# Kernel tuning notes

Measured on AMD Instinct MI355X. Metric: run time of the kernel, lower is better.

## Reference

```python
import jax, jax.numpy as jnp
import numpy as np

N = 100000      # nodes
E = 3200000     # edges (avg degree 32)
NODE, EDGE, H = 11, 2, 32
EPS = 1e-5


def setup_inputs() -> dict:
    key = jax.random.key(0)
    ks = jax.random.split(key, 12)
    def w(k, shape):  # small init like torch Linear
        return jax.random.normal(k, shape, dtype=jnp.float32) * 0.1
    inp = {
        'x': jax.random.normal(ks[0], (N, NODE), dtype=jnp.float32),
        'edge_attr': jax.random.normal(ks[1], (E, EDGE), dtype=jnp.float32),
        'edge_index': jax.random.randint(ks[2], (2, E), 0, N),
        # mlp1: Lin(13,32)-BN-ReLU-Lin(32,32)-BN-ReLU
        'w1a': w(ks[3], (NODE + EDGE, H)), 'b1a': jnp.zeros(H), 'g1a': jnp.ones(H), 'be1a': jnp.zeros(H),
        'w1b': w(ks[4], (H, H)),           'b1b': jnp.zeros(H), 'g1b': jnp.ones(H), 'be1b': jnp.zeros(H),
        # mlp2: Lin(43,32)-BN-ReLU then Lin(32,1)-ReLU (no BN on last)
        'w2a': w(ks[5], (NODE + H, H)), 'b2a': jnp.zeros(H), 'g2a': jnp.ones(H), 'be2a': jnp.zeros(H),
        'w2b': w(ks[6], (H, 1)),        'b2b': jnp.zeros(1),
        # power: Lin(11,32)-BN-ReLU-Lin(32,1)-BN-ReLU
        'wpa': w(ks[7], (NODE, H)), 'bpa': jnp.zeros(H), 'gpa': jnp.ones(H), 'bepa': jnp.zeros(H),
        'wpb': w(ks[8], (H, 1)),    'bpb': jnp.zeros(1), 'gpb': jnp.ones(1), 'bepb': jnp.zeros(1),
    }
    return inp


def _bn(x, g, b):
    # training-mode BatchNorm1d (batch stats, biased variance), like torch default
    mu = x.mean(0, keepdims=True)
    var = ((x - mu) ** 2).mean(0, keepdims=True)
    return (x - mu) * jax.lax.rsqrt(var + EPS) * g + b


def _conv(x, edge_index, edge_attr,
          w1a, b1a, g1a, be1a, w1b, b1b, g1b, be1b,
          w2a, b2a, g2a, be2a, w2b, b2b):
    src, dst = edge_index[0], edge_index[1]
    # message: cat([x_j, edge_attr]) -> mlp1
    m = jnp.concatenate([x[src], edge_attr], axis=1)          # [E, 13]
    m = jax.nn.relu(_bn(m @ w1a + b1a, g1a, be1a))            # [E, 32]
    m = jax.nn.relu(_bn(m @ w1b + b1b, g1b, be1b))            # [E, 32]
    # aggr='max' scatter to destination nodes
    agg = jax.ops.segment_max(m, dst, num_segments=x.shape[0])
    agg = jnp.where(jnp.isneginf(agg), 0.0, agg)              # empty segments -> 0
    # update: cat([x, aggr_out]) -> mlp2, then replace last feature column
    h = jax.nn.relu(_bn(jnp.concatenate([x, agg], axis=1) @ w2a + b2a, g2a, be2a))
    comb = jax.nn.relu(h @ w2b + b2b)                         # [N, 1]
    return jnp.concatenate([x[:, :-1], comb], axis=1)         # [N, 11]


def reference(x, edge_attr, edge_index,
              w1a, b1a, g1a, be1a, w1b, b1b, g1b, be1b,
              w2a, b2a, g2a, be2a, w2b, b2b,
              wpa, bpa, gpa, bepa, wpb, bpb, gpb, bepb):
    for _ in range(3):
        x = _conv(x, edge_index, edge_attr,
                  w1a, b1a, g1a, be1a, w1b, b1b, g1b, be1b,
                  w2a, b2a, g2a, be2a, w2b, b2b)
    h = jax.nn.relu(_bn(x @ wpa + bpa, gpa, bepa))
    out = jax.nn.relu(_bn(h @ wpb + bpb, gpb, bepb))
    return out
```

## Files before the change

kernel.cpp:

```cpp
#include <hip/hip_runtime.h>
#include <hip/hip_bf16.h>
#include <cstddef>

#define NN 100000
#define EE 3200000
#define NBIN 64
static const float EF = 3200000.0f;


__device__ __forceinline__ float wsum(float v) {
  #pragma unroll
  for (int off = 32; off > 0; off >>= 1) v += __shfl_down(v, off, 64);
  return v;
}

__device__ __forceinline__ void reduce64(float sum[32], float ssq[32], float* red,
                                         float* __restrict__ gsum, float* __restrict__ gssq) {
  const int wid = threadIdx.x >> 6, lane = threadIdx.x & 63;
  #pragma unroll
  for (int j = 0; j < 32; j++) {
    float a = wsum(sum[j]);
    float b = wsum(ssq[j]);
    if (lane == 0) { red[wid * 64 + j] = a; red[wid * 64 + 32 + j] = b; }
  }
  __syncthreads();
  if (threadIdx.x < 64) {
    float t = red[threadIdx.x] + red[64 + threadIdx.x] + red[128 + threadIdx.x] + red[192 + threadIdx.x];
    if (threadIdx.x < 32) unsafeAtomicAdd(&gsum[threadIdx.x], t);
    else                  unsafeAtomicAdd(&gssq[threadIdx.x - 32], t);
  }
}

__device__ __forceinline__ void loadrow(const float* __restrict__ xp, int s, float in[13]) {
  const float4* xr = reinterpret_cast<const float4*>(xp + (size_t)s * 12);
  float4 r0 = xr[0], r1 = xr[1], r2 = xr[2];
  in[0]=r0.x; in[1]=r0.y; in[2]=r0.z; in[3]=r0.w; in[4]=r1.x; in[5]=r1.y; in[6]=r1.z; in[7]=r1.w;
  in[8]=r2.x; in[9]=r2.y; in[10]=r2.z;
}

__device__ __forceinline__ unsigned long long packsea(float x, float y) {
  unsigned int xq = (unsigned int)(fmaf(x, 16384.f, 131072.f) + 0.5f);
  unsigned int yq = (unsigned int)(fmaf(y, 16384.f, 131072.f) + 0.5f);
  return (1ULL << 54) | ((unsigned long long)yq << 27) | (unsigned long long)xq;
}


__global__ __launch_bounds__(256) void k_wprep(const float* __restrict__ w1b,
    const float* __restrict__ b1b, const float* __restrict__ g1b,
    const float* __restrict__ w2a, const float* __restrict__ b2a,
    const float* __restrict__ wpa, const float* __restrict__ bpa,
    float* __restrict__ w2tf, float* __restrict__ b1bf,
    float* __restrict__ w2aT, float* __restrict__ wpaT) {
  int t = threadIdx.x;
  for (int i = t; i < 1024; i += 256) {
    int j = i >> 5, k = i & 31;
    float d = (g1b[j] >= 0.f) ? 1.f : -1.f;
    w2tf[j * 32 + k] = d * w1b[k * 32 + j];
  }
  for (int i = t; i < 32 * 43; i += 256) { int j = i & 31, k = i >> 5; w2aT[j * 44 + k] = w2a[k * 32 + j]; }
  for (int i = t; i < 32 * 11; i += 256) { int j = i & 31, k = i >> 5; wpaT[j * 12 + k] = wpa[k * 32 + j]; }
  if (t < 32) {
    float d = (g1b[t] >= 0.f) ? 1.f : -1.f;
    b1bf[t] = d * b1b[t];
    w2aT[t * 44 + 43] = b2a[t];
    wpaT[t * 12 + 11] = bpa[t];
  }
}

__global__ __launch_bounds__(256) void k_prep(const int* __restrict__ dst, const int* __restrict__ src,
    const float* __restrict__ ea, int* __restrict__ cnt, int* __restrict__ rank,
    unsigned long long* __restrict__ nsd, float* __restrict__ cmom) {
  float p0 = 0, p1 = 0, p2 = 0, p3 = 0, p4 = 0;
  const int S = gridDim.x * 256;
  for (int g = blockIdx.x * 256 + threadIdx.x; g < EE / 4; g += S) {
    int4 d4 = reinterpret_cast<const int4*>(dst)[g];
    int4 s4 = reinterpret_cast<const int4*>(src)[g];
    float4 e0 = reinterpret_cast<const float4*>(ea)[2 * g];
    float4 e1 = reinterpret_cast<const float4*>(ea)[2 * g + 1];
    int r0 = atomicAdd(&cnt[d4.x], 1);
    int r1 = atomicAdd(&cnt[d4.y], 1);
    int r2 = atomicAdd(&cnt[d4.z], 1);
    int r3 = atomicAdd(&cnt[d4.w], 1);
    reinterpret_cast<int4*>(rank)[g] = make_int4(r0, r1, r2, r3);
    atomicAdd(&nsd[s4.x], packsea(e0.x, e0.y));
    atomicAdd(&nsd[s4.y], packsea(e0.z, e0.w));
    atomicAdd(&nsd[s4.z], packsea(e1.x, e1.y));
    atomicAdd(&nsd[s4.w], packsea(e1.z, e1.w));
    p0 += e0.x * e0.x + e0.z * e0.z + e1.x * e1.x + e1.z * e1.z;
    p1 += e0.x * e0.y + e0.z * e0.w + e1.x * e1.y + e1.z * e1.w;
    p2 += e0.y * e0.y + e0.w * e0.w + e1.y * e1.y + e1.w * e1.w;
    p3 += e0.x + e0.z + e1.x + e1.z;
    p4 += e0.y + e0.w + e1.y + e1.w;
  }
  p0 = wsum(p0); p1 = wsum(p1); p2 = wsum(p2); p3 = wsum(p3); p4 = wsum(p4);
  if ((threadIdx.x & 63) == 0) {
    unsafeAtomicAdd(&cmom[0], p0); unsafeAtomicAdd(&cmom[1], p1); unsafeAtomicAdd(&cmom[2], p2);
    unsafeAtomicAdd(&cmom[3], p3); unsafeAtomicAdd(&cmom[4], p4);
  }
}

__global__ __launch_bounds__(1024) void k_scan(const int* __restrict__ cnt,
                                               int* __restrict__ starts) {
  __shared__ int part[1024];
  const int T = 1024, CH = (NN + T - 1) / T;
  int t = threadIdx.x;
  int lo = t * CH, hi = min(lo + CH, NN);
  int s = 0;
  for (int i = lo; i < hi; i++) s += cnt[i];
  part[t] = s; __syncthreads();
  for (int off = 1; off < T; off <<= 1) {
    int v = (t >= off) ? part[t - off] : 0;
    __syncthreads();
    part[t] += v;
    __syncthreads();
  }
  int run = part[t] - s;
  for (int i = lo; i < hi; i++) { starts[i] = run; run += cnt[i]; }
  if (t == T - 1) starts[NN] = EE;
}

__global__ __launch_bounds__(256) void k_scatter(const int* __restrict__ dst, const int* __restrict__ src,
    const float* __restrict__ ea, const int* __restrict__ starts, const int* __restrict__ rank,
    int4* __restrict__ edg) {
  const int S = gridDim.x * 256;
  for (int g = blockIdx.x * 256 + threadIdx.x; g < EE / 4; g += S) {
    int4 d4 = reinterpret_cast<const int4*>(dst)[g];
    int4 s4 = reinterpret_cast<const int4*>(src)[g];
    int4 r4 = reinterpret_cast<const int4*>(rank)[g];
    float4 e0 = reinterpret_cast<const float4*>(ea)[2 * g];
    float4 e1 = reinterpret_cast<const float4*>(ea)[2 * g + 1];
    edg[starts[d4.x] + r4.x] = make_int4(s4.x, __float_as_int(e0.x), __float_as_int(e0.y), 0);
    edg[starts[d4.y] + r4.y] = make_int4(s4.y, __float_as_int(e0.z), __float_as_int(e0.w), 0);
    edg[starts[d4.z] + r4.z] = make_int4(s4.z, __float_as_int(e1.x), __float_as_int(e1.y), 0);
    edg[starts[d4.w] + r4.w] = make_int4(s4.w, __float_as_int(e1.z), __float_as_int(e1.w), 0);
  }
}

__global__ __launch_bounds__(256) void k_xp(const float* __restrict__ x, float* __restrict__ xp) {
  int n = blockIdx.x * 256 + threadIdx.x;
  if (n >= NN) return;
  float v[11];
  #pragma unroll
  for (int k = 0; k < 11; k++) v[k] = x[(size_t)n * 11 + k];
  float4* o = reinterpret_cast<float4*>(xp + (size_t)n * 12);
  o[0] = make_float4(v[0], v[1], v[2], v[3]);
  o[1] = make_float4(v[4], v[5], v[6], v[7]);
  o[2] = make_float4(v[8], v[9], v[10], 0.f);
}

__global__ __launch_bounds__(256) void k_mom(const float* __restrict__ xp,
                                             const unsigned long long* __restrict__ nsd,
                                             float* __restrict__ mom) {
  const int n = blockIdx.x * 256 + threadIdx.x;
  const int lane = threadIdx.x & 63;
  float v[11]; float w = 0.f; float sx = 0.f, sy = 0.f;
  #pragma unroll
  for (int k = 0; k < 11; k++) v[k] = 0.f;
  if (n < NN) {
    unsigned long long pv = nsd[n];
    float dg = (float)(unsigned int)(pv >> 54);
    float sxf = (float)(unsigned int)(pv & 0x7FFFFFFull);
    float syf = (float)(unsigned int)((pv >> 27) & 0x7FFFFFFull);
    w = dg;
    sx = sxf * (1.f / 16384.f) - 8.f * dg;
    sy = syf * (1.f / 16384.f) - 8.f * dg;
    loadrow(xp, n, v);
  }
  int ch = 0;
  #pragma unroll
  for (int a = 0; a < 11; a++) {
    float r = wsum(w * v[a]);
    if (lane == 0) unsafeAtomicAdd(&mom[ch], r);
    ch++;
  }
  #pragma unroll
  for (int a = 0; a < 11; a++) {
    #pragma unroll
    for (int b = a; b < 11; b++) {
      float r = wsum(w * v[a] * v[b]);
      if (lane == 0) unsafeAtomicAdd(&mom[ch], r);
      ch++;
    }
  }
  #pragma unroll
  for (int a = 0; a < 11; a++) {
    float rx = wsum(v[a] * sx);
    if (lane == 0) unsafeAtomicAdd(&mom[ch], rx);
    ch++;
    float ry = wsum(v[a] * sy);
    if (lane == 0) unsafeAtomicAdd(&mom[ch], ry);
    ch++;
  }
}

__device__ __forceinline__ float msym(const float* mom, const float* cmom, int k, int l) {
  int a = min(k, l), b = max(k, l);
  if (b < 11) return mom[11 + a * 11 - a * (a - 1) / 2 + (b - a)];
  if (a < 11) return mom[77 + a * 2 + (b - 11)];
  return cmom[(a - 11) + (b - 11)];
}

__global__ void k_fin1(float* __restrict__ mom, const float* __restrict__ cmom,
    const float* __restrict__ w1a, const float* __restrict__ b1a,
    const float* __restrict__ g1a, const float* __restrict__ be1a,
    float* __restrict__ w1f, float* __restrict__ wexy) {
  int j = threadIdx.x;
  float w[13], S[13];
  #pragma unroll
  for (int k = 0; k < 13; k++) w[k] = w1a[k * 32 + j];
  #pragma unroll
  for (int k = 0; k < 11; k++) S[k] = mom[k];
  S[11] = cmom[3]; S[12] = cmom[4];
  float lin = 0.f;
  #pragma unroll
  for (int k = 0; k < 13; k++) lin = fmaf(w[k], S[k], lin);
  float quad = 0.f;
  #pragma unroll
  for (int k = 0; k < 13; k++)
    #pragma unroll
    for (int l = 0; l < 13; l++) quad = fmaf(w[k] * w[l], msym(mom, cmom, k, l), quad);
  const float invE = 1.f / EF;
  float b = b1a[j];
  float mean = fmaf(lin, invE, b);
  float ey2 = (quad + 2.f * b * lin) * invE + b * b;
  float var = fmaxf(ey2 - mean * mean, 0.f);
  float A = g1a[j] * rsqrtf(var + 1e-5f);
  float C = be1a[j] - mean * A;
  #pragma unroll
  for (int k = 0; k < 13; k++) w1f[j * 16 + k] = A * w[k];
  w1f[j * 16 + 13] = fmaf(A, b, C);
  w1f[j * 16 + 14] = 0.f; w1f[j * 16 + 15] = 0.f;
  wexy[j] = A * w[11];
  wexy[32 + j] = A * w[12];
  __syncthreads();
  for (int i = j; i < 128; i += 32) mom[i] = 0.f;
}

__global__ __launch_bounds__(256) void k_P(const float* __restrict__ xp, const float* __restrict__ w1f,
                                           float* __restrict__ P) {
  const int n = blockIdx.x * 256 + threadIdx.x;
  if (n >= NN) return;
  float xv[11];
  loadrow(xp, n, xv);
  float4* op = reinterpret_cast<float4*>(P + (size_t)n * 32);
  #pragma unroll
  for (int jj = 0; jj < 8; jj++) {
    float o[4];
    #pragma unroll
    for (int u = 0; u < 4; u++) {
      int j = 4 * jj + u;
      const float* wr = w1f + j * 16;
      float acc = wr[13];
      #pragma unroll
      for (int k = 0; k < 11; k++) acc = fmaf(xv[k], wr[k], acc);
      o[u] = acc;
    }
    op[jj] = make_float4(o[0], o[1], o[2], o[3]);
  }
}

__global__ __launch_bounds__(256, 6) void k_fusedagg(
    const int* __restrict__ starts, const int4* __restrict__ edg,
    const float* __restrict__ P, const float* __restrict__ wexy,
    const float* __restrict__ w2tf, const float* __restrict__ b1bf,
    float* __restrict__ tzb, float* __restrict__ gms, float* __restrict__ gzq) {
  __shared__ float smx[4][2][32];
  __shared__ float redm[4][32], redq[4][32];
  const int tid = threadIdx.x;
  const int wid = tid >> 6, lane = tid & 63;
  const int half = lane >> 5, l = lane & 31;
  const int c0 = l & 15, h = (l >> 4) & 1;
  const int n = blockIdx.x * 8 + wid * 2 + half;
  const float wex = wexy[l], wey = wexy[32 + l], bz = b1bf[l];
  const float4* wcA = reinterpret_cast<const float4*>(w2tf + (size_t)c0 * 32 + 16 * h);
  const float4* wcB = reinterpret_cast<const float4*>(w2tf + (size_t)(c0 + 16) * 32 + 16 * h);
  const float4 a0 = wcA[0], a1 = wcA[1], a2 = wcA[2], a3 = wcA[3];
  const float4 b0 = wcB[0], b1 = wcB[1], b2 = wcB[2], b3 = wcB[3];
  float tz = -3.0e38f, zq = 0.f, ms = 0.f;
  int lo = 0, hi = 0;
  if (n < NN) { lo = starts[n]; hi = starts[n + 1]; }
  float* msl = &smx[wid][half][0];
  const float* mrd = msl + 16 * h;
  int sl = lo;
  int4 eA = make_int4(0, 0, 0, 0), eB = make_int4(0, 0, 0, 0);
  float pA = 0.f;
  if (sl < hi) {
    eA = edg[sl];
    pA = P[(size_t)eA.x * 32 + l];
  }
  if (sl + 1 < hi) eB = edg[sl + 1];
  while (sl < hi) {
    int4 eC = eB;
    if (sl + 2 < hi) eC = edg[sl + 2];
    float pN = pA;
    if (sl + 1 < hi) pN = P[(size_t)eB.x * 32 + l];
    const float ex = __int_as_float(eA.y), ey = __int_as_float(eA.z);
    const float m = fmaxf(0.f, fmaf(ex, wex, fmaf(ey, wey, pA)));
    ms += m;
    msl[l] = m;
    __builtin_amdgcn_wave_barrier();
    const float4 m0 = *reinterpret_cast<const float4*>(mrd + 0);
    const float4 m1 = *reinterpret_cast<const float4*>(mrd + 4);
    const float4 m2 = *reinterpret_cast<const float4*>(mrd + 8);
    const float4 m3 = *reinterpret_cast<const float4*>(mrd + 12);
    __builtin_amdgcn_wave_barrier();
    float zA0 = 0.f, zA1 = 0.f, zB0 = 0.f, zB1 = 0.f;
    zA0 = fmaf(m0.x, a0.x, zA0); zA1 = fmaf(m0.y, a0.y, zA1);
    zA0 = fmaf(m0.z, a0.z, zA0); zA1 = fmaf(m0.w, a0.w, zA1);
    zA0 = fmaf(m1.x, a1.x, zA0); zA1 = fmaf(m1.y, a1.y, zA1);
    zA0 = fmaf(m1.z, a1.z, zA0); zA1 = fmaf(m1.w, a1.w, zA1);
    zA0 = fmaf(m2.x, a2.x, zA0); zA1 = fmaf(m2.y, a2.y, zA1);
    zA0 = fmaf(m2.z, a2.z, zA0); zA1 = fmaf(m2.w, a2.w, zA1);
    zA0 = fmaf(m3.x, a3.x, zA0); zA1 = fmaf(m3.y, a3.y, zA1);
    zA0 = fmaf(m3.z, a3.z, zA0); zA1 = fmaf(m3.w, a3.w, zA1);
    zB0 = fmaf(m0.x, b0.x, zB0); zB1 = fmaf(m0.y, b0.y, zB1);
    zB0 = fmaf(m0.z, b0.z, zB0); zB1 = fmaf(m0.w, b0.w, zB1);
    zB0 = fmaf(m1.x, b1.x, zB0); zB1 = fmaf(m1.y, b1.y, zB1);
    zB0 = fmaf(m1.z, b1.z, zB0); zB1 = fmaf(m1.w, b1.w, zB1);
    zB0 = fmaf(m2.x, b2.x, zB0); zB1 = fmaf(m2.y, b2.y, zB1);
    zB0 = fmaf(m2.z, b2.z, zB0); zB1 = fmaf(m2.w, b2.w, zB1);
    zB0 = fmaf(m3.x, b3.x, zB0); zB1 = fmaf(m3.y, b3.y, zB1);
    zB0 = fmaf(m3.z, b3.z, zB0); zB1 = fmaf(m3.w, b3.w, zB1);
    float pAh = zA0 + zA1;
    float pBh = zB0 + zB1;
    pAh += __shfl_xor(pAh, 16, 64);
    pBh += __shfl_xor(pBh, 16, 64);
    const float z = ((l & 16) ? pBh : pAh) + bz;
    tz = fmaxf(tz, z);
    zq = fmaf(z, z, zq);
    eA = eB; eB = eC; pA = pN;
    ++sl;
  }
  if (n < NN) tzb[(size_t)n * 32 + l] = tz;
  float msT = ms + __shfl_xor(ms, 32, 64);
  float zqT = zq + __shfl_xor(zq, 32, 64);
  if (lane < 32) { redm[wid][l] = msT; redq[wid][l] = zqT; }
  __syncthreads();
  if (tid < 32) {
    float a = redm[0][tid] + redm[1][tid] + redm[2][tid] + redm[3][tid];
    float b = redq[0][tid] + redq[1][tid] + redq[2][tid] + redq[3][tid];
    const int bin = blockIdx.x & (NBIN - 1);
    unsafeAtomicAdd(&gms[bin * 32 + tid], a);
    unsafeAtomicAdd(&gzq[bin * 32 + tid], b);
  }
}

__global__ void k_fin2(float* __restrict__ gms, float* __restrict__ gzq,
    const float* __restrict__ w1b, const float* __restrict__ b1b,
    const float* __restrict__ g1b, const float* __restrict__ be1b,
    float* __restrict__ A2d, float* __restrict__ C2) {
  __shared__ float sm[32];
  int j = threadIdx.x;
  float msj = 0.f, zqj = 0.f;
  for (int b = 0; b < NBIN; b++) { msj += gms[b * 32 + j]; zqj += gzq[b * 32 + j]; }
  sm[j] = msj;
  __syncthreads();
  float zs = EF * b1b[j];
  #pragma unroll
  for (int k = 0; k < 32; k++) zs = fmaf(w1b[k * 32 + j], sm[k], zs);
  const float invE = 1.f / EF;
  float mu = zs * invE;
  float var = fmaxf(zqj * invE - mu * mu, 0.f);
  float A = g1b[j] * rsqrtf(var + 1e-5f);
  float C = be1b[j] - mu * A;
  float d = (g1b[j] >= 0.f) ? 1.f : -1.f;
  A2d[j] = A * d; C2[j] = C;
  for (int b = 0; b < NBIN; b++) { gms[b * 32 + j] = 0.f; gzq[b * 32 + j] = 0.f; }
}

__global__ void k_finalize(float* __restrict__ sum, float* __restrict__ ssq,
                           const float* __restrict__ g, const float* __restrict__ be,
                           float inv_n, int ncols, float* __restrict__ a, float* __restrict__ c) {
  int j = threadIdx.x;
  if (j < ncols) {
    float mu = sum[j] * inv_n;
    float var = fmaxf(ssq[j] * inv_n - mu * mu, 0.f);
    float s = rsqrtf(var + 1e-5f) * g[j];
    a[j] = s; c[j] = be[j] - mu * s;
    sum[j] = 0.f; ssq[j] = 0.f;
  }
}


__global__ __launch_bounds__(256) void k_hpre2(const float* __restrict__ xp,
    const float* __restrict__ tzb, const int* __restrict__ starts,
    const float* __restrict__ A2d, const float* __restrict__ C2, const float* __restrict__ w2aT,
    float* __restrict__ hpre, float* __restrict__ gsum, float* __restrict__ gssq) {
  __shared__ float red[256];
  const int n = blockIdx.x * 256 + threadIdx.x;
  float h[32], hh[32];
  #pragma unroll
  for (int j = 0; j < 32; j++) h[j] = 0.f;
  if (n < NN) {
    float xv[11];
    loadrow(xp, n, xv);
    const int dg = starts[n + 1] - starts[n];
    float av[32];
    if (dg > 0) {
      const float4* tp = reinterpret_cast<const float4*>(tzb + (size_t)n * 32);
      #pragma unroll
      for (int j = 0; j < 8; j++) {
        float4 v = tp[j];
        av[4 * j]     = fmaxf(0.f, fmaf(A2d[4 * j],     v.x, C2[4 * j]));
        av[4 * j + 1] = fmaxf(0.f, fmaf(A2d[4 * j + 1], v.y, C2[4 * j + 1]));
        av[4 * j + 2] = fmaxf(0.f, fmaf(A2d[4 * j + 2], v.z, C2[4 * j + 2]));
        av[4 * j + 3] = fmaxf(0.f, fmaf(A2d[4 * j + 3], v.w, C2[4 * j + 3]));
      }
    } else {
      #pragma unroll
      for (int j = 0; j < 32; j++) av[j] = 0.f;
    }
    #pragma unroll
    for (int j = 0; j < 32; j++) {
      const float* wr = w2aT + j * 44;
      float acc = wr[43];
      #pragma unroll
      for (int k = 0; k < 11; k++) acc = fmaf(xv[k], wr[k], acc);
      #pragma unroll
      for (int k = 0; k < 32; k++) acc = fmaf(av[k], wr[11 + k], acc);
      h[j] = acc;
    }
    float4* hp = reinterpret_cast<float4*>(hpre + (size_t)n * 32);
    #pragma unroll
    for (int j = 0; j < 8; j++)
      hp[j] = make_float4(h[4 * j], h[4 * j + 1], h[4 * j + 2], h[4 * j + 3]);
  }
  #pragma unroll
  for (int j = 0; j < 32; j++) hh[j] = h[j] * h[j];
  reduce64(h, hh, red, gsum, gssq);
}

__global__ __launch_bounds__(256) void k_comb(const float* __restrict__ hpre,
    const float* __restrict__ a3, const float* __restrict__ c3,
    const float* __restrict__ w2b, const float* __restrict__ b2b, float* __restrict__ xp) {
  const int n = blockIdx.x * 256 + threadIdx.x;
  if (n >= NN) return;
  const float4* hp = reinterpret_cast<const float4*>(hpre + (size_t)n * 32);
  float acc = b2b[0];
  #pragma unroll
  for (int j = 0; j < 8; j++) {
    float4 v = hp[j];
    acc += fmaxf(0.f, fmaf(v.x, a3[4 * j],     c3[4 * j]))     * w2b[4 * j];
    acc += fmaxf(0.f, fmaf(v.y, a3[4 * j + 1], c3[4 * j + 1])) * w2b[4 * j + 1];
    acc += fmaxf(0.f, fmaf(v.z, a3[4 * j + 2], c3[4 * j + 2])) * w2b[4 * j + 2];
    acc += fmaxf(0.f, fmaf(v.w, a3[4 * j + 3], c3[4 * j + 3])) * w2b[4 * j + 3];
  }
  xp[(size_t)n * 12 + 10] = fmaxf(acc, 0.f);
}


__global__ __launch_bounds__(256) void k_p5(const float* __restrict__ xp, const float* __restrict__ wpaT,
                                            float* __restrict__ ybuf,
                                            float* __restrict__ gsum, float* __restrict__ gssq) {
  __shared__ float red[256];
  const int n = blockIdx.x * 256 + threadIdx.x;
  float y[32], yy[32];
  #pragma unroll
  for (int j = 0; j < 32; j++) y[j] = 0.f;
  if (n < NN) {
    float xv[11];
    loadrow(xp, n, xv);
    #pragma unroll
    for (int j = 0; j < 32; j++) {
      const float* wr = wpaT + j * 12;
      float acc = wr[11];
      #pragma unroll
      for (int k = 0; k < 11; k++) acc = fmaf(xv[k], wr[k], acc);
      y[j] = acc;
    }
    float4* yp = reinterpret_cast<float4*>(ybuf + (size_t)n * 32);
    #pragma unroll
    for (int j = 0; j < 8; j++)
      yp[j] = make_float4(y[4 * j], y[4 * j + 1], y[4 * j + 2], y[4 * j + 3]);
  }
  #pragma unroll
  for (int j = 0; j < 32; j++) yy[j] = y[j] * y[j];
  reduce64(y, yy, red, gsum, gssq);
}

__global__ __launch_bounds__(256) void k_p6(const float* __restrict__ ybuf,
    const float* __restrict__ a4, const float* __restrict__ c4,
    const float* __restrict__ wpb, const float* __restrict__ bpb,
    float* __restrict__ yq, float* __restrict__ gsum, float* __restrict__ gssq) {
  __shared__ float red[8];
  const int n = blockIdx.x * 256 + threadIdx.x;
  float sum = 0.f, ssq = 0.f;
  if (n < NN) {
    const float4* yp = reinterpret_cast<const float4*>(ybuf + (size_t)n * 32);
    float q = bpb[0];
    #pragma unroll
    for (int j = 0; j < 8; j++) {
      float4 v = yp[j];
      q = fmaf(fmaxf(0.f, fmaf(v.x, a4[4 * j],     c4[4 * j])),     wpb[4 * j],     q);
      q = fmaf(fmaxf(0.f, fmaf(v.y, a4[4 * j + 1], c4[4 * j + 1])), wpb[4 * j + 1], q);
      q = fmaf(fmaxf(0.f, fmaf(v.z, a4[4 * j + 2], c4[4 * j + 2])), wpb[4 * j + 2], q);
      q = fmaf(fmaxf(0.f, fmaf(v.w, a4[4 * j + 3], c4[4 * j + 3])), wpb[4 * j + 3], q);
    }
    yq[n] = q;
    sum = q; ssq = q * q;
  }
  float s = wsum(sum), qq = wsum(ssq);
  const int wid = threadIdx.x >> 6, lane = threadIdx.x & 63;
  if (lane == 0) { red[wid] = s; red[4 + wid] = qq; }
  __syncthreads();
  if (threadIdx.x == 0) {
    unsafeAtomicAdd(&gsum[0], red[0] + red[1] + red[2] + red[3]);
    unsafeAtomicAdd(&gssq[0], red[4] + red[5] + red[6] + red[7]);
  }
}

__global__ __launch_bounds__(256) void k_p7(const float* __restrict__ yq,
    const float* __restrict__ a5, const float* __restrict__ c5, float* __restrict__ out) {
  int n = blockIdx.x * 256 + threadIdx.x;
  if (n < NN) out[n] = fmaxf(0.f, fmaf(yq[n], a5[0], c5[0]));
}


extern "C" void kernel_launch(void* const* d_in, const int* in_sizes, int n_in,
                              void* d_out, int out_size, void* d_ws, size_t ws_size,
                              hipStream_t stream) {
  const float* x    = (const float*)d_in[0];
  const float* ea   = (const float*)d_in[1];
  const int*   ei   = (const int*)d_in[2];
  const int*   srcp = ei;
  const int*   dstp = ei + EE;
  const float* w1a = (const float*)d_in[3],  *b1a = (const float*)d_in[4];
  const float* g1a = (const float*)d_in[5],  *be1a = (const float*)d_in[6];
  const float* w1b = (const float*)d_in[7],  *b1b = (const float*)d_in[8];
  const float* g1b = (const float*)d_in[9],  *be1b = (const float*)d_in[10];
  const float* w2a = (const float*)d_in[11], *b2a = (const float*)d_in[12];
  const float* g2a = (const float*)d_in[13], *be2a = (const float*)d_in[14];
  const float* w2b = (const float*)d_in[15], *b2b = (const float*)d_in[16];
  const float* wpa = (const float*)d_in[17], *bpa = (const float*)d_in[18];
  const float* gpa = (const float*)d_in[19], *bepa = (const float*)d_in[20];
  const float* wpb = (const float*)d_in[21], *bpb = (const float*)d_in[22];
  const float* gpb = (const float*)d_in[23], *bepb = (const float*)d_in[24];

  size_t off = 0;
  char* base = (char*)d_ws;
  auto alloc = [&](size_t bytes) -> void* {
    void* p = base + off;
    off += (bytes + 255) & ~(size_t)255;
    return p;
  };
  float* stats = (float*)alloc(2048);
  float* coef  = (float*)alloc(2048);
  float* mom   = (float*)alloc(512);
  float* cmom  = (float*)alloc(256);
  float* gmsB  = (float*)alloc(NBIN * 32 * 4);
  float* gzqB  = (float*)alloc(NBIN * 32 * 4);
  float* w1f   = (float*)alloc(16 * 32 * 4);
  float* wexy  = (float*)alloc(64 * 4);
  float* w2tf  = (float*)alloc(32 * 32 * 4);
  float* b1bf  = (float*)alloc(256);
  float* w2aT  = (float*)alloc(32 * 44 * 4);
  float* wpaT  = (float*)alloc(32 * 12 * 4);
  int*   cnt    = (int*)alloc(NN * 4);
  unsigned long long* nsd = (unsigned long long*)alloc((size_t)NN * 8);
  int*   starts = (int*)alloc((NN + 1) * 4);
  int*   rank   = (int*)alloc((size_t)EE * 4);
  int4*  edg    = (int4*)alloc((size_t)EE * 16);
  float* xp     = (float*)alloc((size_t)NN * 12 * 4);
  float* P      = (float*)alloc((size_t)NN * 32 * 4);
  float* tzb    = (float*)alloc((size_t)NN * 32 * 4);
  float* hpre   = (float*)alloc((size_t)NN * 32 * 4);
  float* yq     = (float*)alloc(NN * 4);

  float *SUM3 = stats + 64,  *SSQ3 = stats + 96;
  float *SUM4 = stats + 128, *SSQ4 = stats + 160;
  float *SUM5 = stats + 192, *SSQ5 = stats + 224;
  float *A2d = coef,       *C2 = coef + 32;
  float *A3  = coef + 64,  *C3 = coef + 96;
  float *A4  = coef + 128, *C4 = coef + 160;
  float *A5  = coef + 192, *C5 = coef + 224;

  hipMemsetAsync(stats, 0, 2048, stream);
  hipMemsetAsync(mom, 0, 512 + 256, stream);
  hipMemsetAsync(gmsB, 0, NBIN * 32 * 4 * 2, stream);
  hipMemsetAsync(cnt, 0, NN * 4, stream);
  hipMemsetAsync(nsd, 0, (size_t)NN * 8, stream);

  const int GN = (NN + 255) / 256;
  const int GW = NN / 8;
  const int GE4 = (EE / 4 + 255) / 256;

  k_wprep  <<<1, 256, 0, stream>>>(w1b, b1b, g1b, w2a, b2a, wpa, bpa, w2tf, b1bf, w2aT, wpaT);
  k_prep   <<<GE4, 256, 0, stream>>>(dstp, srcp, ea, cnt, rank, nsd, cmom);
  k_scan   <<<1, 1024, 0, stream>>>(cnt, starts);
  k_scatter<<<GE4, 256, 0, stream>>>(dstp, srcp, ea, starts, rank, edg);
  k_xp     <<<GN, 256, 0, stream>>>(x, xp);

  const float invN = 1.f / (float)NN;
  for (int c = 0; c < 3; c++) {
    k_mom     <<<GN, 256, 0, stream>>>(xp, nsd, mom);
    k_fin1    <<<1, 32, 0, stream>>>(mom, cmom, w1a, b1a, g1a, be1a, w1f, wexy);
    k_P       <<<GN, 256, 0, stream>>>(xp, w1f, P);
    k_fusedagg<<<GW, 256, 0, stream>>>(starts, edg, P, wexy, w2tf, b1bf, tzb, gmsB, gzqB);
    k_fin2    <<<1, 32, 0, stream>>>(gmsB, gzqB, w1b, b1b, g1b, be1b, A2d, C2);
    k_hpre2   <<<GN, 256, 0, stream>>>(xp, tzb, starts, A2d, C2, w2aT, hpre, SUM3, SSQ3);
    k_finalize<<<1, 32, 0, stream>>>(SUM3, SSQ3, g2a, be2a, invN, 32, A3, C3);
    k_comb    <<<GN, 256, 0, stream>>>(hpre, A3, C3, w2b, b2b, xp);
  }

  k_p5      <<<GN, 256, 0, stream>>>(xp, wpaT, hpre, SUM4, SSQ4);
  k_finalize<<<1, 32, 0, stream>>>(SUM4, SSQ4, gpa, bepa, invN, 32, A4, C4);
  k_p6      <<<GN, 256, 0, stream>>>(hpre, A4, C4, wpb, bpb, yq, SUM5, SSQ5);
  k_finalize<<<1, 32, 0, stream>>>(SUM5, SSQ5, gpb, bepb, invN, 1, A5, C5);
  k_p7      <<<GN, 256, 0, stream>>>(yq, A5, C5, (float*)d_out);
}
```

Baseline: 3.969 ms.

## Stage edge records in LDS and process four edges per iteration in fused aggregation

Each half-wave loads up to 32 edge records at once into shared memory, then handles four edges per iteration with the next four gathers of P prefetched, replacing the old one-edge software pipeline. Tail edges are clamped and masked out of the max and sum-of-squares. The aim is more memory-level parallelism on the random P gathers and fewer barriers per edge. In exchange it uses more registers, so launch bounds drop from 6 to 4 blocks per CU, which lowers occupancy.

Measured after the change: 3.995 ms. Within noise of the previous version (+0.6%).

```diff
diff --git a/kernel.cpp b/kernel.cpp
--- a/kernel.cpp
+++ b/kernel.cpp
@@ -259,12 +259,13 @@
   }
 }
 
-__global__ __launch_bounds__(256, 6) void k_fusedagg(
+__global__ __launch_bounds__(256, 4) void k_fusedagg(
     const int* __restrict__ starts, const int4* __restrict__ edg,
     const float* __restrict__ P, const float* __restrict__ wexy,
     const float* __restrict__ w2tf, const float* __restrict__ b1bf,
     float* __restrict__ tzb, float* __restrict__ gms, float* __restrict__ gzq) {
-  __shared__ float smx[4][2][32];
+  __shared__ int4  recl[4][2][32];
+  __shared__ float smx[4][2][4][32];
   __shared__ float redm[4][32], redq[4][32];
   const int tid = threadIdx.x;
   const int wid = tid >> 6, lane = tid & 63;
@@ -279,58 +280,79 @@
   float tz = -3.0e38f, zq = 0.f, ms = 0.f;
   int lo = 0, hi = 0;
   if (n < NN) { lo = starts[n]; hi = starts[n + 1]; }
-  float* msl = &smx[wid][half][0];
-  const float* mrd = msl + 16 * h;
-  int sl = lo;
-  int4 eA = make_int4(0, 0, 0, 0), eB = make_int4(0, 0, 0, 0);
-  float pA = 0.f;
-  if (sl < hi) {
-    eA = edg[sl];
-    pA = P[(size_t)eA.x * 32 + l];
-  }
-  if (sl + 1 < hi) eB = edg[sl + 1];
-  while (sl < hi) {
-    int4 eC = eB;
-    if (sl + 2 < hi) eC = edg[sl + 2];
-    float pN = pA;
-    if (sl + 1 < hi) pN = P[(size_t)eB.x * 32 + l];
-    const float ex = __int_as_float(eA.y), ey = __int_as_float(eA.z);
-    const float m = fmaxf(0.f, fmaf(ex, wex, fmaf(ey, wey, pA)));
-    ms += m;
-    msl[l] = m;
+  int4* recS = &recl[wid][half][0];
+  float (*mS)[32] = smx[wid][half];
+
+#define ZCOMP(D, VALID)                                                           \
+    {                                                                             \
+      const float* mb = &mS[D][16 * h];                                           \
+      const float4 q0 = *reinterpret_cast<const float4*>(mb + 0);                 \
+      const float4 q1 = *reinterpret_cast<const float4*>(mb + 4);                 \
+      const float4 q2 = *reinterpret_cast<const float4*>(mb + 8);                 \
+      const float4 q3 = *reinterpret_cast<const float4*>(mb + 12);                \
+      float zA0 = 0.f, zA1 = 0.f, zB0 = 0.f, zB1 = 0.f;                           \
+      zA0 = fmaf(q0.x, a0.x, zA0); zA1 = fmaf(q0.y, a0.y, zA1);                   \
+      zA0 = fmaf(q0.z, a0.z, zA0); zA1 = fmaf(q0.w, a0.w, zA1);                   \
+      zA0 = fmaf(q1.x, a1.x, zA0); zA1 = fmaf(q1.y, a1.y, zA1);                   \
+      zA0 = fmaf(q1.z, a1.z, zA0); zA1 = fmaf(q1.w, a1.w, zA1);                   \
+      zA0 = fmaf(q2.x, a2.x, zA0); zA1 = fmaf(q2.y, a2.y, zA1);                   \
+      zA0 = fmaf(q2.z, a2.z, zA0); zA1 = fmaf(q2.w, a2.w, zA1);                   \
+      zA0 = fmaf(q3.x, a3.x, zA0); zA1 = fmaf(q3.y, a3.y, zA1);                   \
+      zA0 = fmaf(q3.z, a3.z, zA0); zA1 = fmaf(q3.w, a3.w, zA1);                   \
+      zB0 = fmaf(q0.x, b0.x, zB0); zB1 = fmaf(q0.y, b0.y, zB1);                   \
+      zB0 = fmaf(q0.z, b0.z, zB0); zB1 = fmaf(q0.w, b0.w, zB1);                   \
+      zB0 = fmaf(q1.x, b1.x, zB0); zB1 = fmaf(q1.y, b1.y, zB1);                   \
+      zB0 = fmaf(q1.z, b1.z, zB0); zB1 = fmaf(q1.w, b1.w, zB1);                   \
+      zB0 = fmaf(q2.x, b2.x, zB0); zB1 = fmaf(q2.y, b2.y, zB1);                   \
+      zB0 = fmaf(q2.z, b2.z, zB0); zB1 = fmaf(q2.w, b2.w, zB1);                   \
+      zB0 = fmaf(q3.x, b3.x, zB0); zB1 = fmaf(q3.y, b3.y, zB1);                   \
+      zB0 = fmaf(q3.z, b3.z, zB0); zB1 = fmaf(q3.w, b3.w, zB1);                   \
+      float pAh = zA0 + zA1, pBh = zB0 + zB1;                                     \
+      pAh += __shfl_xor(pAh, 16, 64);                                             \
+      pBh += __shfl_xor(pBh, 16, 64);                                             \
+      const float zz_ = ((l & 16) ? pBh : pAh) + bz;                              \
+      tz = fmaxf(tz, (VALID) ? zz_ : -3.0e38f);                                   \
+      const float zm_ = (VALID) ? zz_ : 0.f;                                      \
+      zq = fmaf(zm_, zm_, zq);                                                    \
+    }
+
+  for (int base = lo; base < hi; base += 32) {
+    const int cnt = min(hi - base, 32);
+    recS[l] = edg[base + (l < cnt ? l : cnt - 1)];
     __builtin_amdgcn_wave_barrier();
-    const float4 m0 = *reinterpret_cast<const float4*>(mrd + 0);
-    const float4 m1 = *reinterpret_cast<const float4*>(mrd + 4);
-    const float4 m2 = *reinterpret_cast<const float4*>(mrd + 8);
-    const float4 m3 = *reinterpret_cast<const float4*>(mrd + 12);
-    __builtin_amdgcn_wave_barrier();
-    float zA0 = 0.f, zA1 = 0.f, zB0 = 0.f, zB1 = 0.f;
-    zA0 = fmaf(m0.x, a0.x, zA0); zA1 = fmaf(m0.y, a0.y, zA1);
-    zA0 = fmaf(m0.z, a0.z, zA0); zA1 = fmaf(m0.w, a0.w, zA1);
-    zA0 = fmaf(m1.x, a1.x, zA0); zA1 = fmaf(m1.y, a1.y, zA1);
-    zA0 = fmaf(m1.z, a1.z, zA0); zA1 = fmaf(m1.w, a1.w, zA1);
-    zA0 = fmaf(m2.x, a2.x, zA0); zA1 = fmaf(m2.y, a2.y, zA1);
-    zA0 = fmaf(m2.z, a2.z, zA0); zA1 = fmaf(m2.w, a2.w, zA1);
-    zA0 = fmaf(m3.x, a3.x, zA0); zA1 = fmaf(m3.y, a3.y, zA1);
-    zA0 = fmaf(m3.z, a3.z, zA0); zA1 = fmaf(m3.w, a3.w, zA1);
-    zB0 = fmaf(m0.x, b0.x, zB0); zB1 = fmaf(m0.y, b0.y, zB1);
-    zB0 = fmaf(m0.z, b0.z, zB0); zB1 = fmaf(m0.w, b0.w, zB1);
-    zB0 = fmaf(m1.x, b1.x, zB0); zB1 = fmaf(m1.y, b1.y, zB1);
-    zB0 = fmaf(m1.z, b1.z, zB0); zB1 = fmaf(m1.w, b1.w, zB1);
-    zB0 = fmaf(m2.x, b2.x, zB0); zB1 = fmaf(m2.y, b2.y, zB1);
-    zB0 = fmaf(m2.z, b2.z, zB0); zB1 = fmaf(m2.w, b2.w, zB1);
-    zB0 = fmaf(m3.x, b3.x, zB0); zB1 = fmaf(m3.y, b3.y, zB1);
-    zB0 = fmaf(m3.z, b3.z, zB0); zB1 = fmaf(m3.w, b3.w, zB1);
-    float pAh = zA0 + zA1;
-    float pBh = zB0 + zB1;
-    pAh += __shfl_xor(pAh, 16, 64);
-    pBh += __shfl_xor(pBh, 16, 64);
-    const float z = ((l & 16) ? pBh : pAh) + bz;
-    tz = fmaxf(tz, z);
-    zq = fmaf(z, z, zq);
-    eA = eB; eB = eC; pA = pN;
-    ++sl;
-  }
+    float pv0 = P[(size_t)recS[0].x * 32 + l];
+    float pv1 = P[(size_t)recS[min(1, cnt - 1)].x * 32 + l];
+    float pv2 = P[(size_t)recS[min(2, cnt - 1)].x * 32 + l];
+    float pv3 = P[(size_t)recS[min(3, cnt - 1)].x * 32 + l];
+    for (int i = 0; i < cnt; i += 4) {
+      float n0 = 0.f, n1 = 0.f, n2 = 0.f, n3 = 0.f;
+      if (i + 4 < cnt) {
+        n0 = P[(size_t)recS[i + 4].x * 32 + l];
+        n1 = P[(size_t)recS[min(i + 5, cnt - 1)].x * 32 + l];
+        n2 = P[(size_t)recS[min(i + 6, cnt - 1)].x * 32 + l];
+        n3 = P[(size_t)recS[min(i + 7, cnt - 1)].x * 32 + l];
+      }
+      const int4 r0 = recS[i];
+      const int4 r1 = recS[min(i + 1, cnt - 1)];
+      const int4 r2 = recS[min(i + 2, cnt - 1)];
+      const int4 r3 = recS[min(i + 3, cnt - 1)];
+      const bool v1 = (i + 1) < cnt, v2 = (i + 2) < cnt, v3 = (i + 3) < cnt;
+      const float m0 = fmaxf(0.f, fmaf(__int_as_float(r0.y), wex, fmaf(__int_as_float(r0.z), wey, pv0)));
+      const float m1 = fmaxf(0.f, fmaf(__int_as_float(r1.y), wex, fmaf(__int_as_float(r1.z), wey, pv1)));
+      const float m2 = fmaxf(0.f, fmaf(__int_as_float(r2.y), wex, fmaf(__int_as_float(r2.z), wey, pv2)));
+      const float m3 = fmaxf(0.f, fmaf(__int_as_float(r3.y), wex, fmaf(__int_as_float(r3.z), wey, pv3)));
+      ms += m0 + (v1 ? m1 : 0.f) + (v2 ? m2 : 0.f) + (v3 ? m3 : 0.f);
+      mS[0][l] = m0; mS[1][l] = m1; mS[2][l] = m2; mS[3][l] = m3;
+      __builtin_amdgcn_wave_barrier();
+      ZCOMP(0, true)
+      ZCOMP(1, v1)
+      ZCOMP(2, v2)
+      ZCOMP(3, v3)
+      __builtin_amdgcn_wave_barrier();
+      pv0 = n0; pv1 = n1; pv2 = n2; pv3 = n3;
+    }
+  }
+#undef ZCOMP
   if (n < NN) tzb[(size_t)n * 32 + l] = tz;
   float msT = ms + __shfl_xor(ms, 32, 64);
   float zqT = zq + __shfl_xor(zq, 32, 64);
```
